# Optimization experiments

Measured on AMD Instinct MI355X. Metric: run time of the kernel, lower is better.

The kernel has to match this reference:

```python
import jax, jax.numpy as jnp
import numpy as np

RADIUS = 0.3
NEIGHBOR_LIMIT = 32
LN_EPS = 1e-5


def setup_inputs() -> dict:
    key = jax.random.key(0)
    k0, k1, k2 = jax.random.split(key, 3)
    N, C = 16384, 256
    pts = jax.random.normal(k0, (N, 3), jnp.float32)
    masks = jnp.ones((N,), dtype=bool)  # all queries active (fixed shape for jit)
    feats = jax.random.normal(k1, (N, C), jnp.float32)
    W = jax.random.normal(k2, (C, C), jnp.float32) * (1.0 / np.sqrt(C))
    b = jnp.zeros((C,), jnp.float32)
    gamma = jnp.ones((C,), jnp.float32)
    beta = jnp.zeros((C,), jnp.float32)
    return {
        "shifted_src_points_c": pts,
        "src_masks": masks,
        "src_feats_c": feats,
        "W": W,
        "b": b,
        "gamma": gamma,
        "beta": beta,
    }


def _ball_query(q, s, radius, k):
    # squared pairwise distances via the ||q||^2 + ||s||^2 - 2 q.s^T identity
    # (avoids the [N, N, 3] broadcast intermediate)
    q2 = jnp.sum(q * q, axis=-1, keepdims=True)        # [Q, 1]
    s2 = jnp.sum(s * s, axis=-1)                        # [N]
    d2 = q2 + s2[None, :] - 2.0 * (q @ s.T)             # [Q, N]
    neg_d2, idx = jax.lax.top_k(-d2, k)                 # k nearest neighbors
    # out-of-radius slots get index 0, matching the original
    # `neighbor_indices[neighbor_indices == N] = 0` padding replacement
    idx = jnp.where(-neg_d2 > radius * radius, 0, idx)
    return idx                                          # [Q, k] int32


def reference(shifted_src_points_c, src_masks, src_feats_c, W, b, gamma, beta):
    # src_masks is all-True by construction -> queries == all points
    q_nodes = shifted_src_points_c
    idx = _ball_query(q_nodes, shifted_src_points_c, RADIUS, NEIGHBOR_LIMIT)
    group = src_feats_c[idx]                            # [Q, K, C] irregular gather
    pooled = jnp.max(group, axis=1)                     # max over neighbors -> [Q, C]
    h = pooled @ W.T + b                                # nn.Linear(256, 256)
    mu = jnp.mean(h, axis=-1, keepdims=True)
    var = jnp.var(h, axis=-1, keepdims=True)
    h = (h - mu) * jax.lax.rsqrt(var + LN_EPS) * gamma + beta  # LayerNorm
    return jax.nn.relu(h)
```

## Files before the change

### kernel.cpp

```cpp
#include <hip/hip_runtime.h>
#include <stdint.h>

#define NPTS 16384
#define CFEAT 256
#define KNN 32
#define RR_HI 0.0900101f
#define NC 34
#define NCELLS (NC * NC * NC)
#define INVW 3.3332222f
#define NBUCK 128

typedef __attribute__((ext_vector_type(8))) short short8;
typedef __attribute__((ext_vector_type(4))) float floatx4;

__device__ __forceinline__ uint32_t f2bf(uint32_t u) {
  return (u + 0x7fffu + ((u >> 16) & 1u)) >> 16;
}
__device__ __forceinline__ int cell1d(float x) {
  int c = (int)floorf((x + 5.1f) * INVW);
  return min(max(c, 0), NC - 1);
}

__global__ __launch_bounds__(256) void k_cvt(const float* __restrict__ src,
                                             uint16_t* __restrict__ dst, int n4) {
  int i = blockIdx.x * 256 + threadIdx.x;
  if (i >= n4) return;
  uint4 u = ((const uint4*)src)[i];
  uint32_t lo = f2bf(u.x) | (f2bf(u.y) << 16);
  uint32_t hi = f2bf(u.z) | (f2bf(u.w) << 16);
  ((uint2*)dst)[i] = make_uint2(lo, hi);
}

__global__ __launch_bounds__(256) void k_hist(const float* __restrict__ pts,
                                              uint32_t* __restrict__ cellcnt) {
  const int i = blockIdx.x * 256 + threadIdx.x;
  const int cx = cell1d(pts[3 * i]), cy = cell1d(pts[3 * i + 1]), cz = cell1d(pts[3 * i + 2]);
  atomicAdd(&cellcnt[(cz * NC + cy) * NC + cx], 1u);
}

__global__ __launch_bounds__(1024) void k_scan(const uint32_t* __restrict__ hist,
                                               uint32_t* __restrict__ start, int n) {
  __shared__ uint32_t wsum[16];
  __shared__ uint32_t carry;
  const int t = threadIdx.x, wv = t >> 6, ln = t & 63;
  if (t == 0) carry = 0;
  __syncthreads();
  const int nq = n >> 2;
  for (int qb = 0; qb < nq; qb += 1024) {
    const int i4 = qb + t;
    uint4 v = make_uint4(0, 0, 0, 0);
    if (i4 < nq) v = ((const uint4*)hist)[i4];
    const uint32_t tot = v.x + v.y + v.z + v.w;
    uint32_t s = tot;
    #pragma unroll
    for (int off = 1; off < 64; off <<= 1) {
      uint32_t o = __shfl_up(s, off, 64);
      if (ln >= off) s += o;
    }
    if (ln == 63) wsum[wv] = s;
    const uint32_t cbase = carry;
    __syncthreads();
    uint32_t woff = 0;
    for (int w = 0; w < wv; ++w) woff += wsum[w];
    if (i4 < nq) {
      const uint32_t e = cbase + woff + s - tot;
      ((uint4*)start)[i4] = make_uint4(e, e + v.x, e + v.x + v.y, e + v.x + v.y + v.z);
    }
    __syncthreads();
    if (t == 1023) carry = cbase + woff + s;
    __syncthreads();
  }
  if (t == 0) start[n] = carry;
}

__global__ __launch_bounds__(256) void k_scatter(const float* __restrict__ pts,
                                                 const uint32_t* __restrict__ cellstart,
                                                 uint32_t* __restrict__ cellptr,
                                                 uint32_t* __restrict__ sortedq,
                                                 float4* __restrict__ sortedpts) {
  const int i = blockIdx.x * 256 + threadIdx.x;
  const float x = pts[3 * i], y = pts[3 * i + 1], z = pts[3 * i + 2];
  const int c = (cell1d(z) * NC + cell1d(y)) * NC + cell1d(x);
  const uint32_t pos = cellstart[c] + atomicAdd(&cellptr[c], 1u);
  sortedq[pos] = (uint32_t)i;
  sortedpts[pos] = make_float4(x, y, z, __uint_as_float((uint32_t)i));
}

__global__ __launch_bounds__(256) void k_fsp(const uint32_t* __restrict__ sortedq,
                                             const uint32_t* __restrict__ cellstart,
                                             const float4* __restrict__ sortedpts,
                                             const uint16_t* __restrict__ featsb,
                                             uint16_t* __restrict__ pooledb) {
  __shared__ uint64_t keys[4][256];
  __shared__ uint32_t hist[4][NBUCK];
  __shared__ uint32_t sids[4][KNN];
  const int t = threadIdx.x;
  const int w = t >> 6;
  const int lane = t & 63;
  const uint64_t ltmask = (1ull << lane) - 1ull;
  const int q = (int)sortedq[blockIdx.x * 4 + w];
  const float qx = sortedpts[blockIdx.x * 4 + w].x;
  const float qy = sortedpts[blockIdx.x * 4 + w].y;
  const float qz = sortedpts[blockIdx.x * 4 + w].z;
  const int icx = cell1d(qx), icy = cell1d(qy), icz = cell1d(qz);
  const int x0 = max(icx - 1, 0), x1 = min(icx + 1, NC - 1);
  uint32_t c_run = 0;
  #pragma unroll
  for (int dz = -1; dz <= 1; ++dz) {
    const int cz = icz + dz;
    if (cz < 0 || cz >= NC) continue;
    #pragma unroll
    for (int dy = -1; dy <= 1; ++dy) {
      const int cy = icy + dy;
      if (cy < 0 || cy >= NC) continue;
      const int rb = (cz * NC + cy) * NC;
      const int s = (int)cellstart[rb + x0];
      const int e = (int)cellstart[rb + x1 + 1];
      for (int base = s; base < e; base += 64) {
        const int i = base + lane;
        const int ii = (i < e) ? i : (e - 1);
        const float4 p = sortedpts[ii];
        const float dxf = qx - p.x, dyf = qy - p.y, dzf = qz - p.z;
        const float d2 = __fmaf_rn(dxf, dxf, __fmaf_rn(dyf, dyf, __fmul_rn(dzf, dzf)));
        bool pass = (i < e) && (d2 <= RR_HI);
        uint64_t key = 0;
        if (pass) {
          const double ddx = (double)qx - (double)p.x;
          const double ddy = (double)qy - (double)p.y;
          const double ddz = (double)qz - (double)p.z;
          const double dd2 = fma(ddx, ddx, fma(ddy, ddy, ddz * ddz));
          pass = (dd2 <= 0.3 * 0.3);
          key = ((uint64_t)__double_as_longlong(dd2) & ~0x3FFFull) |
                (uint64_t)__float_as_uint(p.w);
        }
        const uint64_t mask = __ballot(pass);
        if (pass) {
          const uint32_t pos = c_run + (uint32_t)__popcll(mask & ltmask);
          if (pos < 256u) keys[w][pos] = key;
        }
        c_run += (uint32_t)__popcll(mask);
      }
    }
  }
  const int c = (int)min(c_run, 256u);
  if (c <= KNN) {
    if (lane < KNN) sids[w][lane] = (lane < c) ? (uint32_t)(keys[w][lane] & 0x3FFFull) : 0u;
  } else {
    const uint64_t INVALID = ~0ull;
    uint64_t k0 = (lane < c) ? keys[w][lane] : INVALID;
    uint64_t k1 = (lane + 64 < c) ? keys[w][lane + 64] : INVALID;
    uint64_t k2 = (lane + 128 < c) ? keys[w][lane + 128] : INVALID;
    uint64_t k3 = (lane + 192 < c) ? keys[w][lane + 192] : INVALID;
    hist[w][lane] = 0;
    hist[w][lane + 64] = 0;
    int b0 = 999, b1 = 999, b2 = 999, b3 = 999;
    const float bs = 128.0f / 0.09f;
    if (k0 != INVALID) { b0 = min(NBUCK - 1, (int)((float)__longlong_as_double((long long)(k0 & ~0x3FFFull)) * bs)); atomicAdd(&hist[w][b0], 1u); }
    if (k1 != INVALID) { b1 = min(NBUCK - 1, (int)((float)__longlong_as_double((long long)(k1 & ~0x3FFFull)) * bs)); atomicAdd(&hist[w][b1], 1u); }
    if (k2 != INVALID) { b2 = min(NBUCK - 1, (int)((float)__longlong_as_double((long long)(k2 & ~0x3FFFull)) * bs)); atomicAdd(&hist[w][b2], 1u); }
    if (k3 != INVALID) { b3 = min(NBUCK - 1, (int)((float)__longlong_as_double((long long)(k3 & ~0x3FFFull)) * bs)); atomicAdd(&hist[w][b3], 1u); }
    const uint32_t h0 = hist[w][2 * lane], h1 = hist[w][2 * lane + 1];
    const uint32_t tot = h0 + h1;
    uint32_t s = tot;
    #pragma unroll
    for (int off = 1; off < 64; off <<= 1) {
      uint32_t o = __shfl_up(s, off, 64);
      if (lane >= off) s += o;
    }
    const uint32_t C0 = s - tot + h0;
    const uint32_t C1 = s - tot + h0 + h1;
    const uint64_t me = __ballot(C0 >= KNN);
    const uint64_t mo = __ballot(C1 >= KNN);
    const int be = me ? 2 * (__ffsll((unsigned long long)me) - 1) : (1 << 30);
    const int bo = mo ? 2 * (__ffsll((unsigned long long)mo) - 1) + 1 : (1 << 30);
    const int bstar = min(be, bo);
    const uint32_t mval_mine = (bstar & 1) ? (C1 - h1) : (C0 - h0);
    const uint32_t m = (uint32_t)__shfl((int)mval_mine, bstar >> 1, 64);
    uint32_t wpos = 0;
    {
      bool win = (b0 < bstar);
      uint64_t bm = __ballot(win);
      if (win) sids[w][wpos + (uint32_t)__popcll(bm & ltmask)] = (uint32_t)(k0 & 0x3FFFull);
      wpos += (uint32_t)__popcll(bm);
      win = (b1 < bstar); bm = __ballot(win);
      if (win) sids[w][wpos + (uint32_t)__popcll(bm & ltmask)] = (uint32_t)(k1 & 0x3FFFull);
      wpos += (uint32_t)__popcll(bm);
      win = (b2 < bstar); bm = __ballot(win);
      if (win) sids[w][wpos + (uint32_t)__popcll(bm & ltmask)] = (uint32_t)(k2 & 0x3FFFull);
      wpos += (uint32_t)__popcll(bm);
      win = (b3 < bstar); bm = __ballot(win);
      if (win) sids[w][wpos + (uint32_t)__popcll(bm & ltmask)] = (uint32_t)(k3 & 0x3FFFull);
      wpos += (uint32_t)__popcll(bm);
    }
    uint64_t e0 = (b0 == bstar) ? k0 : INVALID;
    uint64_t e1 = (b1 == bstar) ? k1 : INVALID;
    uint64_t e2 = (b2 == bstar) ? k2 : INVALID;
    uint64_t e3 = (b3 == bstar) ? k3 : INVALID;
    const int need = KNN - (int)m;
    for (int it = 0; it < need; ++it) {
      uint64_t a = e0 < e1 ? e0 : e1;
      uint64_t b = e2 < e3 ? e2 : e3;
      uint64_t mn = a < b ? a : b;
      #pragma unroll
      for (int off = 1; off < 64; off <<= 1) {
        uint64_t o = (uint64_t)__shfl_xor((unsigned long long)mn, off, 64);
        mn = o < mn ? o : mn;
      }
      if (e0 == mn) e0 = INVALID;
      else if (e1 == mn) e1 = INVALID;
      else if (e2 == mn) e2 = INVALID;
      else if (e3 == mn) e3 = INVALID;
      if (lane == 0) sids[w][m + it] = (uint32_t)(mn & 0x3FFFull);
    }
  }
  float m0 = -3.0e38f, m1 = -3.0e38f, m2 = -3.0e38f, m3 = -3.0e38f;
  #pragma unroll 8
  for (int k = 0; k < KNN; ++k) {
    const uint32_t idx = sids[w][k];
    const uint2 v = *(const uint2*)(featsb + (size_t)idx * CFEAT + lane * 4);
    m0 = fmaxf(m0, __uint_as_float(v.x << 16));
    m1 = fmaxf(m1, __uint_as_float(v.x & 0xffff0000u));
    m2 = fmaxf(m2, __uint_as_float(v.y << 16));
    m3 = fmaxf(m3, __uint_as_float(v.y & 0xffff0000u));
  }
  const uint32_t lo = (__float_as_uint(m0) >> 16) | (__float_as_uint(m1) & 0xffff0000u);
  const uint32_t hi = (__float_as_uint(m2) >> 16) | (__float_as_uint(m3) & 0xffff0000u);
  ((uint2*)pooledb)[(size_t)q * 64 + lane] = make_uint2(lo, hi);
}

__global__ __launch_bounds__(256) void k_gemm_ln(const uint16_t* __restrict__ pooledb,
                                                 const uint16_t* __restrict__ Wb,
                                                 const float* __restrict__ bias,
                                                 const float* __restrict__ gamma,
                                                 const float* __restrict__ beta,
                                                 float* __restrict__ out) {
  __shared__ uint16_t As[64 * 264];
  __shared__ uint16_t Bs[256 * 40];
  __shared__ float red1[4][64];
  __shared__ float red2[4][64];
  __shared__ float mu_s[64];
  __shared__ float rs_s[64];
  const int t = threadIdx.x;
  const int wave = t >> 6;
  const int lane = t & 63;
  const int quad = lane >> 4;
  const int l15 = lane & 15;
  const int m0 = blockIdx.x * 64;
  {
    const int m = t >> 2, qtr = t & 3;
    const uint4* src = (const uint4*)(pooledb + (size_t)(m0 + m) * 256 + qtr * 64);
    uint4* dst = (uint4*)(As + m * 264 + qtr * 64);
    #pragma unroll
    for (int i = 0; i < 8; ++i) dst[i] = src[i];
  }
  floatx4 acc[4][4];
  #pragma unroll
  for (int mi = 0; mi < 4; ++mi)
    #pragma unroll
    for (int ni = 0; ni < 4; ++ni)
      acc[mi][ni] = (floatx4){0.f, 0.f, 0.f, 0.f};

  for (int step = 0; step < 8; ++step) {
    __syncthreads();
    {
      const uint4* src = (const uint4*)(Wb + (size_t)t * 256 + step * 32);
      uint4* dst = (uint4*)(Bs + t * 40);
      #pragma unroll
      for (int i = 0; i < 4; ++i) dst[i] = src[i];
    }
    __syncthreads();
    short8 a[4], b[4];
    #pragma unroll
    for (int mi = 0; mi < 4; ++mi)
      a[mi] = *(const short8*)(As + (mi * 16 + l15) * 264 + step * 32 + quad * 8);
    #pragma unroll
    for (int ni = 0; ni < 4; ++ni)
      b[ni] = *(const short8*)(Bs + (wave * 64 + ni * 16 + l15) * 40 + quad * 8);
    #pragma unroll
    for (int mi = 0; mi < 4; ++mi)
      #pragma unroll
      for (int ni = 0; ni < 4; ++ni)
        acc[mi][ni] = __builtin_amdgcn_mfma_f32_16x16x32_bf16(a[mi], b[ni], acc[mi][ni], 0, 0, 0);
  }

  float bcol[4], gcol[4], zcol[4];
  #pragma unroll
  for (int ni = 0; ni < 4; ++ni) {
    const int col = wave * 64 + ni * 16 + l15;
    bcol[ni] = bias[col];
    gcol[ni] = gamma[col];
    zcol[ni] = beta[col];
  }
  #pragma unroll
  for (int mi = 0; mi < 4; ++mi)
    #pragma unroll
    for (int ni = 0; ni < 4; ++ni)
      #pragma unroll
      for (int r = 0; r < 4; ++r)
        acc[mi][ni][r] += bcol[ni];
  #pragma unroll
  for (int mi = 0; mi < 4; ++mi) {
    #pragma unroll
    for (int r = 0; r < 4; ++r) {
      const float v0 = acc[mi][0][r], v1 = acc[mi][1][r], v2 = acc[mi][2][r], v3 = acc[mi][3][r];
      float s1 = v0 + v1 + v2 + v3;
      float s2 = v0 * v0 + v1 * v1 + v2 * v2 + v3 * v3;
      #pragma unroll
      for (int off = 1; off < 16; off <<= 1) {
        s1 += __shfl_xor(s1, off, 64);
        s2 += __shfl_xor(s2, off, 64);
      }
      if (l15 == 0) {
        const int row = mi * 16 + quad * 4 + r;
        red1[wave][row] = s1;
        red2[wave][row] = s2;
      }
    }
  }
  __syncthreads();
  if (t < 64) {
    const float s1 = red1[0][t] + red1[1][t] + red1[2][t] + red1[3][t];
    const float s2 = red2[0][t] + red2[1][t] + red2[2][t] + red2[3][t];
    const float mu = s1 * (1.0f / 256.0f);
    const float var = s2 * (1.0f / 256.0f) - mu * mu;
    mu_s[t] = mu;
    rs_s[t] = 1.0f / sqrtf(var + 1e-5f);
  }
  __syncthreads();
  #pragma unroll
  for (int mi = 0; mi < 4; ++mi) {
    #pragma unroll
    for (int r = 0; r < 4; ++r) {
      const int row = mi * 16 + quad * 4 + r;
      const float mu = mu_s[row], rs = rs_s[row];
      #pragma unroll
      for (int ni = 0; ni < 4; ++ni) {
        float y = (acc[mi][ni][r] - mu) * rs * gcol[ni] + zcol[ni];
        out[(size_t)(m0 + row) * 256 + wave * 64 + ni * 16 + l15] = fmaxf(y, 0.0f);
      }
    }
  }
}

extern "C" void kernel_launch(void* const* d_in, const int* in_sizes, int n_in,
                              void* d_out, int out_size, void* d_ws, size_t ws_size,
                              hipStream_t stream) {
  (void)in_sizes; (void)n_in; (void)out_size; (void)ws_size;
  const float* pts   = (const float*)d_in[0];
  const float* feats = (const float*)d_in[2];
  const float* Wm    = (const float*)d_in[3];
  const float* bias  = (const float*)d_in[4];
  const float* gamma = (const float*)d_in[5];
  const float* beta  = (const float*)d_in[6];
  float* out = (float*)d_out;

  uint8_t* ws = (uint8_t*)d_ws;
  uint16_t* featsb    = (uint16_t*)ws;
  uint16_t* Wb        = (uint16_t*)(ws + 8388608);
  uint16_t* pooledb   = (uint16_t*)(ws + 8519680);
  uint32_t* cellcnt   = (uint32_t*)(ws + 16908288);
  uint32_t* cellptr   = (uint32_t*)(ws + 17065728);
  uint32_t* cellstart = (uint32_t*)(ws + 17223168);
  uint32_t* sortedq   = (uint32_t*)(ws + 17380608);
  float4*   sortedpts = (float4*)(ws + 17446144);

  (void)hipMemsetAsync(cellcnt, 0, 2 * 157440, stream);
  k_cvt<<<4096, 256, 0, stream>>>(feats, featsb, NPTS * CFEAT / 4);
  k_cvt<<<64, 256, 0, stream>>>(Wm, Wb, CFEAT * CFEAT / 4);
  k_hist<<<NPTS / 256, 256, 0, stream>>>(pts, cellcnt);
  k_scan<<<1, 1024, 0, stream>>>(cellcnt, cellstart, NCELLS);
  k_scatter<<<NPTS / 256, 256, 0, stream>>>(pts, cellstart, cellptr, sortedq, sortedpts);
  k_fsp<<<NPTS / 4, 256, 0, stream>>>(sortedq, cellstart, sortedpts, featsb, pooledb);
  k_gemm_ln<<<NPTS / 64, 256, 0, stream>>>(pooledb, Wb, bias, gamma, beta, out);
}
```

Before: 155.8 us.

## Fuse prep kernels, widen scan per thread, flatten neighbor-cell iteration

Merges the two bf16 conversion kernels and the cell histogram into a single launch, with the histogram piggybacking on the 64 weight-conversion blocks. The scan now handles four uint4 per thread, so it needs far fewer serial iterations and barriers. The neighbor search in k_fsp flattens its nine cell-row ranges into one virtual index space, so each wavefront iteration covers neighbors across row boundaries instead of running partially filled 64-lane chunks per row. The flattening adds a per-lane select chain to compute each address, and the histogram is now served by only 64 blocks.

```diff
diff --git a/kernel.cpp b/kernel.cpp
--- a/kernel.cpp
+++ b/kernel.cpp
@@ -21,21 +21,28 @@
   return min(max(c, 0), NC - 1);
 }
 
-__global__ __launch_bounds__(256) void k_cvt(const float* __restrict__ src,
-                                             uint16_t* __restrict__ dst, int n4) {
-  int i = blockIdx.x * 256 + threadIdx.x;
-  if (i >= n4) return;
-  uint4 u = ((const uint4*)src)[i];
-  uint32_t lo = f2bf(u.x) | (f2bf(u.y) << 16);
-  uint32_t hi = f2bf(u.z) | (f2bf(u.w) << 16);
-  ((uint2*)dst)[i] = make_uint2(lo, hi);
-}
-
-__global__ __launch_bounds__(256) void k_hist(const float* __restrict__ pts,
+__global__ __launch_bounds__(256) void k_prep(const float* __restrict__ feats,
+                                              uint16_t* __restrict__ featsb,
+                                              const float* __restrict__ Wm,
+                                              uint16_t* __restrict__ Wb,
+                                              const float* __restrict__ pts,
                                               uint32_t* __restrict__ cellcnt) {
-  const int i = blockIdx.x * 256 + threadIdx.x;
-  const int cx = cell1d(pts[3 * i]), cy = cell1d(pts[3 * i + 1]), cz = cell1d(pts[3 * i + 2]);
-  atomicAdd(&cellcnt[(cz * NC + cy) * NC + cx], 1u);
+  const int b = blockIdx.x, t = threadIdx.x;
+  if (b < 4096) {
+    const int i = b * 256 + t;
+    const uint4 u = ((const uint4*)feats)[i];
+    const uint32_t lo = f2bf(u.x) | (f2bf(u.y) << 16);
+    const uint32_t hi = f2bf(u.z) | (f2bf(u.w) << 16);
+    ((uint2*)featsb)[i] = make_uint2(lo, hi);
+  } else {
+    const int i = (b - 4096) * 256 + t;
+    const uint4 u = ((const uint4*)Wm)[i];
+    const uint32_t lo = f2bf(u.x) | (f2bf(u.y) << 16);
+    const uint32_t hi = f2bf(u.z) | (f2bf(u.w) << 16);
+    ((uint2*)Wb)[i] = make_uint2(lo, hi);
+    const int cx = cell1d(pts[3 * i]), cy = cell1d(pts[3 * i + 1]), cz = cell1d(pts[3 * i + 2]);
+    atomicAdd(&cellcnt[(cz * NC + cy) * NC + cx], 1u);
+  }
 }
 
 __global__ __launch_bounds__(1024) void k_scan(const uint32_t* __restrict__ hist,
@@ -46,11 +53,17 @@
   if (t == 0) carry = 0;
   __syncthreads();
   const int nq = n >> 2;
-  for (int qb = 0; qb < nq; qb += 1024) {
-    const int i4 = qb + t;
-    uint4 v = make_uint4(0, 0, 0, 0);
-    if (i4 < nq) v = ((const uint4*)hist)[i4];
-    const uint32_t tot = v.x + v.y + v.z + v.w;
+  for (int qb = 0; qb < nq; qb += 4096) {
+    uint4 v[4];
+    uint32_t psum[4];
+    uint32_t tot = 0;
+    #pragma unroll
+    for (int k = 0; k < 4; ++k) {
+      const int i4 = qb + t * 4 + k;
+      v[k] = (i4 < nq) ? ((const uint4*)hist)[i4] : make_uint4(0, 0, 0, 0);
+      psum[k] = tot;
+      tot += v[k].x + v[k].y + v[k].z + v[k].w;
+    }
     uint32_t s = tot;
     #pragma unroll
     for (int off = 1; off < 64; off <<= 1) {
@@ -62,12 +75,18 @@
     __syncthreads();
     uint32_t woff = 0;
     for (int w = 0; w < wv; ++w) woff += wsum[w];
-    if (i4 < nq) {
-      const uint32_t e = cbase + woff + s - tot;
-      ((uint4*)start)[i4] = make_uint4(e, e + v.x, e + v.x + v.y, e + v.x + v.y + v.z);
+    const uint32_t base = cbase + woff + s - tot;
+    #pragma unroll
+    for (int k = 0; k < 4; ++k) {
+      const int i4 = qb + t * 4 + k;
+      if (i4 < nq) {
+        const uint32_t e = base + psum[k];
+        ((uint4*)start)[i4] =
+            make_uint4(e, e + v[k].x, e + v[k].x + v[k].y, e + v[k].x + v[k].y + v[k].z);
+      }
     }
     __syncthreads();
-    if (t == 1023) carry = cbase + woff + s;
+    if (t == 1023) carry = base + tot;
     __syncthreads();
   }
   if (t == 0) start[n] = carry;
@@ -99,48 +118,57 @@
   const int lane = t & 63;
   const uint64_t ltmask = (1ull << lane) - 1ull;
   const int q = (int)sortedq[blockIdx.x * 4 + w];
-  const float qx = sortedpts[blockIdx.x * 4 + w].x;
-  const float qy = sortedpts[blockIdx.x * 4 + w].y;
-  const float qz = sortedpts[blockIdx.x * 4 + w].z;
+  const float4 qp = sortedpts[blockIdx.x * 4 + w];
+  const float qx = qp.x, qy = qp.y, qz = qp.z;
   const int icx = cell1d(qx), icy = cell1d(qy), icz = cell1d(qz);
   const int x0 = max(icx - 1, 0), x1 = min(icx + 1, NC - 1);
+  int S[9], E[9];
+  #pragma unroll
+  for (int r = 0; r < 9; ++r) {
+    const int cz = icz + (r / 3) - 1;
+    const int cy = icy + (r % 3) - 1;
+    const bool ok = (cz >= 0) && (cz < NC) && (cy >= 0) && (cy < NC);
+    const int rb = ((ok ? cz : 0) * NC + (ok ? cy : 0)) * NC;
+    const int s = (int)cellstart[rb + x0];
+    const int e = (int)cellstart[rb + x1 + 1];
+    S[r] = ok ? s : 0;
+    E[r] = ok ? e : 0;
+  }
+  int PRE[10], OFF[9];
+  PRE[0] = 0;
+  #pragma unroll
+  for (int r = 0; r < 9; ++r) {
+    PRE[r + 1] = PRE[r] + (E[r] - S[r]);
+    OFF[r] = S[r] - PRE[r];
+  }
+  const int total = PRE[9];
   uint32_t c_run = 0;
-  #pragma unroll
-  for (int dz = -1; dz <= 1; ++dz) {
-    const int cz = icz + dz;
-    if (cz < 0 || cz >= NC) continue;
-    #pragma unroll
-    for (int dy = -1; dy <= 1; ++dy) {
-      const int cy = icy + dy;
-      if (cy < 0 || cy >= NC) continue;
-      const int rb = (cz * NC + cy) * NC;
-      const int s = (int)cellstart[rb + x0];
-      const int e = (int)cellstart[rb + x1 + 1];
-      for (int base = s; base < e; base += 64) {
-        const int i = base + lane;
-        const int ii = (i < e) ? i : (e - 1);
-        const float4 p = sortedpts[ii];
-        const float dxf = qx - p.x, dyf = qy - p.y, dzf = qz - p.z;
-        const float d2 = __fmaf_rn(dxf, dxf, __fmaf_rn(dyf, dyf, __fmul_rn(dzf, dzf)));
-        bool pass = (i < e) && (d2 <= RR_HI);
-        uint64_t key = 0;
-        if (pass) {
-          const double ddx = (double)qx - (double)p.x;
-          const double ddy = (double)qy - (double)p.y;
-          const double ddz = (double)qz - (double)p.z;
-          const double dd2 = fma(ddx, ddx, fma(ddy, ddy, ddz * ddz));
-          pass = (dd2 <= 0.3 * 0.3);
-          key = ((uint64_t)__double_as_longlong(dd2) & ~0x3FFFull) |
-                (uint64_t)__float_as_uint(p.w);
-        }
-        const uint64_t mask = __ballot(pass);
-        if (pass) {
-          const uint32_t pos = c_run + (uint32_t)__popcll(mask & ltmask);
-          if (pos < 256u) keys[w][pos] = key;
-        }
-        c_run += (uint32_t)__popcll(mask);
-      }
-    }
+  for (int v0 = 0; v0 < total; v0 += 64) {
+    const int v = v0 + lane;
+    int addr = v + OFF[0];
+    #pragma unroll
+    for (int r = 1; r < 9; ++r) addr = (v >= PRE[r]) ? (v + OFF[r]) : addr;
+    const int ia = min(addr, NPTS - 1);
+    const float4 p = sortedpts[ia];
+    const float dxf = qx - p.x, dyf = qy - p.y, dzf = qz - p.z;
+    const float d2 = __fmaf_rn(dxf, dxf, __fmaf_rn(dyf, dyf, __fmul_rn(dzf, dzf)));
+    bool pass = (v < total) && (d2 <= RR_HI);
+    uint64_t key = 0;
+    if (pass) {
+      const double ddx = (double)qx - (double)p.x;
+      const double ddy = (double)qy - (double)p.y;
+      const double ddz = (double)qz - (double)p.z;
+      const double dd2 = fma(ddx, ddx, fma(ddy, ddy, ddz * ddz));
+      pass = (dd2 <= 0.3 * 0.3);
+      key = ((uint64_t)__double_as_longlong(dd2) & ~0x3FFFull) |
+            (uint64_t)__float_as_uint(p.w);
+    }
+    const uint64_t mask = __ballot(pass);
+    if (pass) {
+      const uint32_t pos = c_run + (uint32_t)__popcll(mask & ltmask);
+      if (pos < 256u) keys[w][pos] = key;
+    }
+    c_run += (uint32_t)__popcll(mask);
   }
   const int c = (int)min(c_run, 256u);
   if (c <= KNN) {
@@ -365,11 +393,9 @@
   float4*   sortedpts = (float4*)(ws + 17446144);
 
   (void)hipMemsetAsync(cellcnt, 0, 2 * 157440, stream);
-  k_cvt<<<4096, 256, 0, stream>>>(feats, featsb, NPTS * CFEAT / 4);
-  k_cvt<<<64, 256, 0, stream>>>(Wm, Wb, CFEAT * CFEAT / 4);
-  k_hist<<<NPTS / 256, 256, 0, stream>>>(pts, cellcnt);
+  k_prep<<<4160, 256, 0, stream>>>(feats, featsb, Wm, Wb, pts, cellcnt);
   k_scan<<<1, 1024, 0, stream>>>(cellcnt, cellstart, NCELLS);
-  k_scatter<<<NPTS / 256, 256, 0, stream>>>(pts, cellstart, cellptr, sortedq, sortedpts);
-  k_fsp<<<NPTS / 4, 256, 0, stream>>>(sortedq, cellstart, sortedpts, featsb, pooledb);
-  k_gemm_ln<<<NPTS / 64, 256, 0, stream>>>(pooledb, Wb, bias, gamma, beta, out);
-}
+  k_scatter<<<64, 256, 0, stream>>>(pts, cellstart, cellptr, sortedq, sortedpts);
+  k_fsp<<<4096, 256, 0, stream>>>(sortedq, cellstart, sortedpts, featsb, pooledb);
+  k_gemm_ln<<<256, 256, 0, stream>>>(pooledb, Wb, bias, gamma, beta, out);
+}
```

Measured after the change: 145.8 us. -6.4%, faster.
